# Optimization experiments

Hardware: AMD Instinct MI355X
Metric: run time of the kernel (lower is better)

## Reference

```python
import jax, jax.numpy as jnp
import numpy as np

E = 512   # embed_dim
H = 16    # num_heads
D = E // H  # head_dim = 32
L = 2048  # target (query) length
S = 2048  # source (stored pattern) length
N = 4     # batch
LN_EPS = 1e-5


def setup_inputs() -> dict:
    key = jax.random.key(0)
    ks = jax.random.split(key, 8)
    inv_sqrt_e = 1.0 / np.sqrt(E).astype(np.float32)
    return {
        "query": jax.random.normal(ks[0], (L, N, E), jnp.float32),
        "key_in": jax.random.normal(ks[1], (S, N, E), jnp.float32),
        "value": jax.random.normal(ks[2], (S, N, E), jnp.float32),
        "scaling": jax.random.uniform(ks[3], (H,), jnp.float32),  # per-head beta
        "in_proj_weight": jax.random.normal(ks[4], (3 * E, E), jnp.float32) * inv_sqrt_e,
        "in_proj_bias": jnp.zeros((3 * E,), jnp.float32),
        "p_norm_weight": jnp.ones((D,), jnp.float32),
        "p_norm_bias": jnp.zeros((D,), jnp.float32),
        "out_proj_weight": jax.random.normal(ks[5], (E, E), jnp.float32) * inv_sqrt_e,
        "out_proj_bias": jnp.zeros((E,), jnp.float32),
    }


def reference(query, key_in, value, scaling, in_proj_weight, in_proj_bias,
              p_norm_weight, p_norm_bias, out_proj_weight, out_proj_bias):
    Lq, Nb, Ed = query.shape
    Sk = key_in.shape[0]
    # split packed in-projection (torch Linear convention: y = x @ W^T + b)
    wq, wk, wv = jnp.split(in_proj_weight, 3, axis=0)
    bq, bk, bv = jnp.split(in_proj_bias, 3, axis=0)
    q = jnp.einsum('lne,fe->lnf', query, wq) + bq
    k = jnp.einsum('sne,fe->snf', key_in, wk) + bk
    v = jnp.einsum('sne,fe->snf', value, wv) + bv
    # (len, N, H*D) -> (N, H, len, D)
    q = q.reshape(Lq, Nb, H, D).transpose(1, 2, 0, 3)
    k = k.reshape(Sk, Nb, H, D).transpose(1, 2, 0, 3)
    v = v.reshape(Sk, Nb, H, D).transpose(1, 2, 0, 3)

    def pattern_norm(x):
        # affine LayerNorm over the association (head) dimension D
        mu = jnp.mean(x, axis=-1, keepdims=True)
        var = jnp.mean(jnp.square(x - mu), axis=-1, keepdims=True)
        return (x - mu) * jax.lax.rsqrt(var + LN_EPS) * p_norm_weight + p_norm_bias

    k = pattern_norm(k)
    v = pattern_norm(v)

    beta = scaling.reshape(1, H, 1, 1)  # per-head inverse-temperature
    scores = jnp.einsum('nhld,nhsd->nhls', q * beta, k)  # [N,H,L,S]
    attn = jax.nn.softmax(scores, axis=-1)  # single Hopfield update (update_steps_max=0)
    out = jnp.einsum('nhls,nhsd->nhld', attn, v)  # [N,H,L,D]
    out = out.transpose(2, 0, 1, 3).reshape(Lq, Nb, H * D)
    out = jnp.einsum('lnf,of->lno', out, out_proj_weight) + out_proj_bias
    return out  # (L, N, E)
```

## Files before the change

kernel.cpp:

```cpp
#include <hip/hip_runtime.h>
#include <cstdint>

#define LN_EPS 1e-5f

typedef _Float16 f16;
typedef _Float16 half4_t __attribute__((ext_vector_type(4)));
typedef _Float16 half8_t __attribute__((ext_vector_type(8)));
typedef __fp16 fp16v2 __attribute__((ext_vector_type(2)));
typedef float f32x4 __attribute__((ext_vector_type(4)));

__device__ __forceinline__ void gl_lds16(const void* g, void* l) {
    __builtin_amdgcn_global_load_lds(
        (__attribute__((address_space(1))) void*)(uintptr_t)g,
        (__attribute__((address_space(3))) void*)(uint32_t)(uintptr_t)l,
        16, 0, 0);
}

__device__ __forceinline__ half4_t pack4(float a, float b, float c, float d) {
    fp16v2 lo = __builtin_amdgcn_cvt_pkrtz(a, b);
    fp16v2 hi = __builtin_amdgcn_cvt_pkrtz(c, d);
    half4_t r;
    r[0] = (f16)lo[0]; r[1] = (f16)lo[1]; r[2] = (f16)hi[0]; r[3] = (f16)hi[1];
    return r;
}

__global__ void k_cast(const float* __restrict__ W1f, const float* __restrict__ W2f,
                       f16* __restrict__ W1h, f16* __restrict__ W2h) {
    int t = blockIdx.x * blockDim.x + threadIdx.x;
    const int n1 = (1536 * 512) / 4;
    const float4* src;
    half4_t* dst;
    int idx;
    if (t < n1) { src = (const float4*)W1f; dst = (half4_t*)W1h; idx = t; }
    else        { src = (const float4*)W2f; dst = (half4_t*)W2h; idx = t - n1; }
    float4 v = src[idx];
    half4_t h;
    h[0] = (f16)v.x; h[1] = (f16)v.y; h[2] = (f16)v.z; h[3] = (f16)v.w;
    dst[idx] = h;
}

__global__ __launch_bounds__(256) void k_inproj(
    const float* __restrict__ Xq, const float* __restrict__ Xk, const float* __restrict__ Xv,
    const f16* __restrict__ W1, const float* __restrict__ bias,
    const float* __restrict__ scaling,
    f16* __restrict__ Qg, f16* __restrict__ Kg, f16* __restrict__ Vg)
{
    __shared__ __align__(16) f16 Al[128 * 32];
    __shared__ __align__(16) f16 Bl[128 * 32];

    const int tid = threadIdx.x;
    const int m0 = blockIdx.x * 128;
    const int f0 = blockIdx.y * 128;
    const int sec = f0 >> 9;
    const float* X = (sec == 0) ? Xq : ((sec == 1) ? Xk : Xv);
    f16* Ob = (sec == 0) ? Qg : ((sec == 1) ? Kg : Vg);
    const int fl0 = f0 & 511;

    const int wid = tid >> 6, ln = tid & 63, l15 = ln & 15, quad = ln >> 4;
    const int wm = wid >> 1, wn = wid & 1;

    f32x4 z4 = {0.f, 0.f, 0.f, 0.f};
    f32x4 acc[4][4];
    #pragma unroll
    for (int i = 0; i < 4; ++i)
        #pragma unroll
        for (int j = 0; j < 4; ++j) acc[i][j] = z4;

    for (int kt = 0; kt < 16; ++kt) {
        const int k0 = kt * 32;
        #pragma unroll
        for (int i = 0; i < 2; ++i) {
            int row = wid * 32 + i * 16 + (ln >> 2);
            gl_lds16(W1 + (size_t)(f0 + row) * 512 + k0 + (ln & 3) * 8,
                     Bl + (wid * 32 + i * 16) * 32);
        }
        #pragma unroll
        for (int c = 0; c < 4; ++c) {
            int ch = c * 256 + tid;
            int row = ch >> 3, q4 = ch & 7;
            float4 v = *(const float4*)(X + (size_t)(m0 + row) * 512 + k0 + q4 * 4);
            *(half4_t*)(Al + row * 32 + q4 * 4) = pack4(v.x, v.y, v.z, v.w);
        }
        __syncthreads();

        half8_t a[4], b[4];
        #pragma unroll
        for (int i = 0; i < 4; ++i)
            a[i] = *(const half8_t*)(Al + (wm * 64 + i * 16 + l15) * 32 + quad * 8);
        #pragma unroll
        for (int j = 0; j < 4; ++j)
            b[j] = *(const half8_t*)(Bl + (wn * 64 + j * 16 + l15) * 32 + quad * 8);
        #pragma unroll
        for (int i = 0; i < 4; ++i)
            #pragma unroll
            for (int j = 0; j < 4; ++j)
                acc[i][j] = __builtin_amdgcn_mfma_f32_16x16x32_f16(a[i], b[j], acc[i][j], 0, 0, 0);
        __syncthreads();
    }

    #pragma unroll
    for (int i = 0; i < 4; ++i) {
        int row = m0 + wm * 64 + i * 16 + quad * 4;
        #pragma unroll
        for (int j = 0; j < 4; ++j) {
            int col = wn * 64 + j * 16 + l15;
            int f_local = fl0 + col;
            int hh = f_local >> 5, cc = (f_local >> 3) & 3, e = f_local & 7;
            float bs = bias[f0 + col];
            float sc2 = (sec == 0) ? scaling[hh] * 1.44269504f : 1.0f;
            #pragma unroll
            for (int r = 0; r < 4; ++r) {
                int rm = row + r;
                int l = rm >> 2, nb = rm & 3;
                int gg = nb * 16 + hh;
                Ob[(size_t)gg * 65536 + (size_t)cc * 16384 + (size_t)l * 8 + e] =
                    (f16)((acc[i][j][r] + bs) * sc2);
            }
        }
    }
}

__global__ void k_norm_k(f16* __restrict__ Kg, const float* __restrict__ w,
                         const float* __restrict__ b) {
    int t = blockIdx.x * 256 + threadIdx.x;
    int g = t >> 11, s = t & 2047;
    f16* base = Kg + (size_t)g * 65536 + (size_t)s * 8;
    half8_t x[4];
    float xf[32], s1 = 0.f, s2 = 0.f;
    #pragma unroll
    for (int c = 0; c < 4; ++c) {
        x[c] = *(const half8_t*)(base + (size_t)c * 16384);
        #pragma unroll
        for (int j = 0; j < 8; ++j) {
            float v = (float)x[c][j];
            xf[c * 8 + j] = v; s1 += v; s2 += v * v;
        }
    }
    float mean = s1 * (1.f / 32.f);
    float var = s2 * (1.f / 32.f) - mean * mean;
    float rs = rsqrtf(var + LN_EPS);
    #pragma unroll
    for (int c = 0; c < 4; ++c) {
        half8_t y;
        #pragma unroll
        for (int j = 0; j < 8; ++j) {
            int d = c * 8 + j;
            y[j] = (f16)((xf[d] - mean) * rs * w[d] + b[d]);
        }
        *(half8_t*)(base + (size_t)c * 16384) = y;
    }
}

__global__ void k_norm_vt(const f16* __restrict__ Vg, const float* __restrict__ w,
                          const float* __restrict__ b, f16* __restrict__ Vtg) {
    __shared__ __align__(16) f16 T[32 * 64];
    const int t = threadIdx.x;
    const int seg = blockIdx.x, g = blockIdx.y;
    const int s_l = t >> 2, c = t & 3;
    half8_t v = *(const half8_t*)(Vg + (size_t)g * 65536 + (size_t)c * 16384 +
                                  (size_t)(seg * 64 + s_l) * 8);
    float xf[8], s1 = 0.f, s2 = 0.f;
    #pragma unroll
    for (int j = 0; j < 8; ++j) { xf[j] = (float)v[j]; s1 += xf[j]; s2 += xf[j] * xf[j]; }
    s1 += __shfl_xor(s1, 1); s1 += __shfl_xor(s1, 2);
    s2 += __shfl_xor(s2, 1); s2 += __shfl_xor(s2, 2);
    float mean = s1 * (1.f / 32.f);
    float var = s2 * (1.f / 32.f) - mean * mean;
    float rs = rsqrtf(var + LN_EPS);
    int cs = s_l >> 3, es = s_l & 7;
    #pragma unroll
    for (int j = 0; j < 8; ++j) {
        int d = c * 8 + j;
        T[d * 64 + (cs ^ j) * 8 + es] = (f16)((xf[j] - mean) * rs * w[d] + b[d]);
    }
    __syncthreads();
    int d_o = t >> 3, c_o = t & 7;
    half8_t out = *(const half8_t*)(T + d_o * 64 + c_o * 8);
    *(half8_t*)(Vtg + (size_t)(g * 32 + seg) * 2048 + d_o * 64 + c_o * 8) = out;
}

__global__ __launch_bounds__(256, 4) void k_flash(
    const f16* __restrict__ Qg, const f16* __restrict__ Kg,
    const f16* __restrict__ Vtg, f16* __restrict__ Og)
{
    __shared__ __align__(16) char smem[26624];
    f16* Kl = (f16*)smem;
    char* VtB = smem + 4096;
    char* PlAll = smem + 8192;

    const int tid = threadIdx.x, wid = tid >> 6, ln = tid & 63;
    const int l15 = ln & 15, quad = ln >> 4;
    char* Pw = PlAll + wid * 4608;
    const int g = blockIdx.y, h = g & 15, n = g >> 4;
    const int q0 = blockIdx.x * 128;

    #pragma unroll
    for (int ii = 0; ii < 2; ++ii)
        gl_lds16(Qg + (size_t)g * 65536 + (size_t)wid * 16384 + (size_t)(q0 + ii * 64) * 8 + ln * 8,
                 PlAll + wid * 2048 + ii * 1024);
    __syncthreads();
    half8_t aq[2];
    #pragma unroll
    for (int i = 0; i < 2; ++i)
        aq[i] = *(const half8_t*)(PlAll + quad * 2048 + (wid * 32 + i * 16 + l15) * 16);

    f32x4 z4 = {0.f, 0.f, 0.f, 0.f};
    f32x4 accO[2][2];
    accO[0][0] = z4; accO[0][1] = z4; accO[1][0] = z4; accO[1][1] = z4;
    float m_i[2] = {-1e30f, -1e30f}, l_i[2] = {0.f, 0.f};

    for (int st = 0; st < 32; ++st) {
        __syncthreads();
        gl_lds16(Kg + (size_t)g * 65536 + (size_t)wid * 16384 + (size_t)(st * 64) * 8 + ln * 8,
                 (char*)Kl + wid * 1024);
        gl_lds16(Vtg + (size_t)(g * 32 + st) * 2048 + wid * 512 + ln * 8,
                 VtB + wid * 1024);
        __syncthreads();

        half8_t ak[4];
        #pragma unroll
        for (int mt = 0; mt < 4; ++mt)
            ak[mt] = *(const half8_t*)((char*)Kl + quad * 1024 + (mt * 16 + l15) * 16);
        f32x4 accS[2][4];
        #pragma unroll
        for (int i = 0; i < 2; ++i)
            #pragma unroll
            for (int mt = 0; mt < 4; ++mt)
                accS[i][mt] = __builtin_amdgcn_mfma_f32_16x16x32_f16(ak[mt], aq[i], z4, 0, 0, 0);

        #pragma unroll
        for (int i = 0; i < 2; ++i) {
            float xmax = accS[i][0][0];
            #pragma unroll
            for (int mt = 0; mt < 4; ++mt)
                #pragma unroll
                for (int r = 0; r < 4; ++r) xmax = fmaxf(xmax, accS[i][mt][r]);
            xmax = fmaxf(xmax, __shfl_xor(xmax, 16));
            xmax = fmaxf(xmax, __shfl_xor(xmax, 32));
            float mnew = fmaxf(m_i[i], xmax);
            float alpha = __builtin_amdgcn_exp2f(m_i[i] - mnew);
            float rs = 0.f;
            #pragma unroll
            for (int mt = 0; mt < 4; ++mt) {
                float p0 = __builtin_amdgcn_exp2f(accS[i][mt][0] - mnew);
                float p1 = __builtin_amdgcn_exp2f(accS[i][mt][1] - mnew);
                float p2 = __builtin_amdgcn_exp2f(accS[i][mt][2] - mnew);
                float p3 = __builtin_amdgcn_exp2f(accS[i][mt][3] - mnew);
                rs += (p0 + p1) + (p2 + p3);
                *(half4_t*)(Pw + (i * 16 + l15) * 144 + mt * 32 + quad * 8) =
                    pack4(p0, p1, p2, p3);
            }
            rs += __shfl_xor(rs, 16);
            rs += __shfl_xor(rs, 32);
            l_i[i] = l_i[i] * alpha + rs;
            m_i[i] = mnew;
            #pragma unroll
            for (int dt = 0; dt < 2; ++dt)
                #pragma unroll
                for (int r = 0; r < 4; ++r) accO[i][dt][r] *= alpha;
        }

        #pragma unroll
        for (int kt = 0; kt < 2; ++kt) {
            half8_t av[2], bp[2];
            #pragma unroll
            for (int dt = 0; dt < 2; ++dt) {
                int d = dt * 16 + l15;
                int cp = (kt * 4 + quad) ^ (l15 & 7);
                av[dt] = *(const half8_t*)(VtB + d * 128 + cp * 16);
            }
            #pragma unroll
            for (int i = 0; i < 2; ++i)
                bp[i] = *(const half8_t*)(Pw + (i * 16 + l15) * 144 + kt * 64 + quad * 16);
            #pragma unroll
            for (int i = 0; i < 2; ++i)
                #pragma unroll
                for (int dt = 0; dt < 2; ++dt)
                    accO[i][dt] = __builtin_amdgcn_mfma_f32_16x16x32_f16(av[dt], bp[i], accO[i][dt], 0, 0, 0);
        }
    }

    #pragma unroll
    for (int i = 0; i < 2; ++i) {
        float inv = 1.f / l_i[i];
        #pragma unroll
        for (int dt = 0; dt < 2; ++dt) {
            *(half4_t*)(Pw + (i * 16 + l15) * 80 + (dt * 16 + quad * 4) * 2) =
                pack4(accO[i][dt][0] * inv, accO[i][dt][1] * inv,
                      accO[i][dt][2] * inv, accO[i][dt][3] * inv);
        }
    }
    int q2 = ln >> 1, hf = ln & 1;
    half8_t o0 = *(const half8_t*)(Pw + q2 * 80 + hf * 32);
    half8_t o1 = *(const half8_t*)(Pw + q2 * 80 + hf * 32 + 16);
    size_t rowe = ((size_t)(n * 2048 + q0 + wid * 32 + q2)) * 512 + h * 32 + hf * 16;
    *(half8_t*)(Og + rowe) = o0;
    *(half8_t*)(Og + rowe + 8) = o1;
}

__global__ __launch_bounds__(256) void k_outproj(
    const f16* __restrict__ A, const f16* __restrict__ W2,
    const float* __restrict__ bias, float* __restrict__ Out)
{
    __shared__ __align__(16) f16 Al[128 * 32];
    __shared__ __align__(16) f16 Bl[128 * 32];

    const int tid = threadIdx.x;
    const int m0 = blockIdx.x * 128;
    const int f0 = blockIdx.y * 128;
    const int wid = tid >> 6, ln = tid & 63, l15 = ln & 15, quad = ln >> 4;
    const int wm = wid >> 1, wn = wid & 1;

    f32x4 z4 = {0.f, 0.f, 0.f, 0.f};
    f32x4 acc[4][4];
    #pragma unroll
    for (int i = 0; i < 4; ++i)
        #pragma unroll
        for (int j = 0; j < 4; ++j) acc[i][j] = z4;

    for (int kt = 0; kt < 16; ++kt) {
        const int k0 = kt * 32;
        #pragma unroll
        for (int i = 0; i < 2; ++i) {
            int row = wid * 32 + i * 16 + (ln >> 2);
            gl_lds16(A + (size_t)(m0 + row) * 512 + k0 + (ln & 3) * 8,
                     Al + (wid * 32 + i * 16) * 32);
            gl_lds16(W2 + (size_t)(f0 + row) * 512 + k0 + (ln & 3) * 8,
                     Bl + (wid * 32 + i * 16) * 32);
        }
        __syncthreads();

        half8_t a[4], b[4];
        #pragma unroll
        for (int i = 0; i < 4; ++i)
            a[i] = *(const half8_t*)(Al + (wm * 64 + i * 16 + l15) * 32 + quad * 8);
        #pragma unroll
        for (int j = 0; j < 4; ++j)
            b[j] = *(const half8_t*)(Bl + (wn * 64 + j * 16 + l15) * 32 + quad * 8);
        #pragma unroll
        for (int i = 0; i < 4; ++i)
            #pragma unroll
            for (int j = 0; j < 4; ++j)
                acc[i][j] = __builtin_amdgcn_mfma_f32_16x16x32_f16(a[i], b[j], acc[i][j], 0, 0, 0);
        __syncthreads();
    }

    #pragma unroll
    for (int i = 0; i < 4; ++i) {
        int row = m0 + wm * 64 + i * 16 + quad * 4;
        #pragma unroll
        for (int j = 0; j < 4; ++j) {
            int col = wn * 64 + j * 16 + l15;
            float bs = bias[f0 + col];
            #pragma unroll
            for (int r = 0; r < 4; ++r) {
                int rm = row + r;
                int orow = (rm & 2047) * 4 + (rm >> 11);
                Out[(size_t)orow * 512 + f0 + col] = acc[i][j][r] + bs;
            }
        }
    }
}

extern "C" void kernel_launch(void* const* d_in, const int* in_sizes, int n_in,
                              void* d_out, int out_size, void* d_ws, size_t ws_size,
                              hipStream_t stream) {
    const float* query   = (const float*)d_in[0];
    const float* key_in  = (const float*)d_in[1];
    const float* value   = (const float*)d_in[2];
    const float* scaling = (const float*)d_in[3];
    const float* ipw     = (const float*)d_in[4];
    const float* ipb     = (const float*)d_in[5];
    const float* pnw     = (const float*)d_in[6];
    const float* pnb     = (const float*)d_in[7];
    const float* opw     = (const float*)d_in[8];
    const float* opb     = (const float*)d_in[9];
    float* out = (float*)d_out;

    f16* Qg  = (f16*)d_ws;
    f16* Kg  = Qg  + (size_t)4194304;
    f16* Vg  = Kg  + (size_t)4194304;
    f16* Vtg = Vg  + (size_t)4194304;
    f16* W1  = Vtg + (size_t)4194304;
    f16* W2  = W1  + (size_t)786432;
    f16* Og  = Vg;

    k_cast<<<1024, 256, 0, stream>>>(ipw, opw, W1, W2);
    k_inproj<<<dim3(64, 12), 256, 0, stream>>>(query, key_in, value, W1, ipb, scaling, Qg, Kg, Vg);
    k_norm_k<<<512, 256, 0, stream>>>(Kg, pnw, pnb);
    k_norm_vt<<<dim3(32, 64), 256, 0, stream>>>(Vg, pnw, pnb, Vtg);
    k_flash<<<dim3(16, 64), 256, 0, stream>>>(Qg, Kg, Vtg, Og);
    k_outproj<<<dim3(64, 4), 256, 0, stream>>>(Og, W2, opb, out);
}
```

Measured before the change: 244.6 us.

## Double-buffer K/V tiles in flash kernel, halve query tile, vectorize GEMM epilogues

The flash-attention kernel now handles 64 queries per block instead of 128, which doubles the grid and raises the occupancy hint to 6. It also double-buffers the K and V^T tiles in LDS, prefetching the next tile with global_load_lds while computing on the current one, so one barrier per iteration replaces two. In the in-projection and out-projection GEMMs the MFMA operands are swapped, letting each lane hold 4 consecutive output columns and write vectorized half4/float4 stores with a float4 bias load. The risk is that smaller query tiles reload K/V more often, which adds L2 traffic.

```diff
diff --git a/kernel.cpp b/kernel.cpp
--- a/kernel.cpp
+++ b/kernel.cpp
@@ -34,9 +34,7 @@
     if (t < n1) { src = (const float4*)W1f; dst = (half4_t*)W1h; idx = t; }
     else        { src = (const float4*)W2f; dst = (half4_t*)W2h; idx = t - n1; }
     float4 v = src[idx];
-    half4_t h;
-    h[0] = (f16)v.x; h[1] = (f16)v.y; h[2] = (f16)v.z; h[3] = (f16)v.w;
-    dst[idx] = h;
+    dst[idx] = pack4(v.x, v.y, v.z, v.w);
 }
 
 __global__ __launch_bounds__(256) void k_inproj(
@@ -94,28 +92,26 @@
         for (int i = 0; i < 4; ++i)
             #pragma unroll
             for (int j = 0; j < 4; ++j)
-                acc[i][j] = __builtin_amdgcn_mfma_f32_16x16x32_f16(a[i], b[j], acc[i][j], 0, 0, 0);
-        __syncthreads();
-    }
-
-    #pragma unroll
-    for (int i = 0; i < 4; ++i) {
-        int row = m0 + wm * 64 + i * 16 + quad * 4;
-        #pragma unroll
-        for (int j = 0; j < 4; ++j) {
-            int col = wn * 64 + j * 16 + l15;
-            int f_local = fl0 + col;
-            int hh = f_local >> 5, cc = (f_local >> 3) & 3, e = f_local & 7;
-            float bs = bias[f0 + col];
-            float sc2 = (sec == 0) ? scaling[hh] * 1.44269504f : 1.0f;
-            #pragma unroll
-            for (int r = 0; r < 4; ++r) {
-                int rm = row + r;
-                int l = rm >> 2, nb = rm & 3;
-                int gg = nb * 16 + hh;
-                Ob[(size_t)gg * 65536 + (size_t)cc * 16384 + (size_t)l * 8 + e] =
-                    (f16)((acc[i][j][r] + bs) * sc2);
-            }
+                acc[i][j] = __builtin_amdgcn_mfma_f32_16x16x32_f16(b[j], a[i], acc[i][j], 0, 0, 0);
+        __syncthreads();
+    }
+
+    #pragma unroll
+    for (int j = 0; j < 4; ++j) {
+        int fb = f0 + wn * 64 + j * 16;
+        int floc = (fb & 511) + quad * 4;
+        int hh = floc >> 5;
+        int cc = (floc >> 3) & 3, e0 = floc & 7;
+        float sc2 = (sec == 0) ? scaling[hh] * 1.44269504f : 1.0f;
+        float4 bs4 = *(const float4*)(bias + fb + quad * 4);
+        #pragma unroll
+        for (int i = 0; i < 4; ++i) {
+            int rm = m0 + wm * 64 + i * 16 + l15;
+            int l = rm >> 2, nb = rm & 3;
+            int gg = nb * 16 + hh;
+            *(half4_t*)(Ob + (size_t)gg * 65536 + (size_t)cc * 16384 + (size_t)l * 8 + e0) =
+                pack4((acc[i][j][0] + bs4.x) * sc2, (acc[i][j][1] + bs4.y) * sc2,
+                      (acc[i][j][2] + bs4.z) * sc2, (acc[i][j][3] + bs4.w) * sc2);
         }
     }
 }
@@ -179,123 +175,109 @@
     *(half8_t*)(Vtg + (size_t)(g * 32 + seg) * 2048 + d_o * 64 + c_o * 8) = out;
 }
 
-__global__ __launch_bounds__(256, 4) void k_flash(
+__global__ __launch_bounds__(256, 6) void k_flash(
     const f16* __restrict__ Qg, const f16* __restrict__ Kg,
     const f16* __restrict__ Vtg, f16* __restrict__ Og)
 {
-    __shared__ __align__(16) char smem[26624];
-    f16* Kl = (f16*)smem;
-    char* VtB = smem + 4096;
-    char* PlAll = smem + 8192;
+    __shared__ __align__(16) char smem[25600];
 
     const int tid = threadIdx.x, wid = tid >> 6, ln = tid & 63;
     const int l15 = ln & 15, quad = ln >> 4;
-    char* Pw = PlAll + wid * 4608;
+    char* Pw = smem + 16384 + wid * 2304;
     const int g = blockIdx.y, h = g & 15, n = g >> 4;
-    const int q0 = blockIdx.x * 128;
-
-    #pragma unroll
-    for (int ii = 0; ii < 2; ++ii)
-        gl_lds16(Qg + (size_t)g * 65536 + (size_t)wid * 16384 + (size_t)(q0 + ii * 64) * 8 + ln * 8,
-                 PlAll + wid * 2048 + ii * 1024);
+    const int q0 = blockIdx.x * 64;
+
+    gl_lds16(Qg + (size_t)g * 65536 + (size_t)wid * 16384 + (size_t)(q0 + ln) * 8,
+             smem + 16384 + wid * 1024);
+    gl_lds16(Kg + (size_t)g * 65536 + (size_t)wid * 16384 + (size_t)ln * 8,
+             smem + wid * 1024);
+    gl_lds16(Vtg + (size_t)(g * 32 + 0) * 2048 + wid * 512 + ln * 8,
+             smem + 8192 + wid * 1024);
+    __builtin_amdgcn_s_waitcnt(0x0F70);
     __syncthreads();
-    half8_t aq[2];
-    #pragma unroll
-    for (int i = 0; i < 2; ++i)
-        aq[i] = *(const half8_t*)(PlAll + quad * 2048 + (wid * 32 + i * 16 + l15) * 16);
+    half8_t aq = *(const half8_t*)(smem + 16384 + quad * 1024 + (wid * 16 + l15) * 16);
 
     f32x4 z4 = {0.f, 0.f, 0.f, 0.f};
-    f32x4 accO[2][2];
-    accO[0][0] = z4; accO[0][1] = z4; accO[1][0] = z4; accO[1][1] = z4;
-    float m_i[2] = {-1e30f, -1e30f}, l_i[2] = {0.f, 0.f};
+    f32x4 accO[2];
+    accO[0] = z4; accO[1] = z4;
+    float m_i = -1e30f, l_i = 0.f;
 
     for (int st = 0; st < 32; ++st) {
-        __syncthreads();
-        gl_lds16(Kg + (size_t)g * 65536 + (size_t)wid * 16384 + (size_t)(st * 64) * 8 + ln * 8,
-                 (char*)Kl + wid * 1024);
-        gl_lds16(Vtg + (size_t)(g * 32 + st) * 2048 + wid * 512 + ln * 8,
-                 VtB + wid * 1024);
-        __syncthreads();
+        const int cur = st & 1, nxt = cur ^ 1;
+        if (st < 31) {
+            gl_lds16(Kg + (size_t)g * 65536 + (size_t)wid * 16384 + (size_t)((st + 1) * 64 + ln) * 8,
+                     smem + nxt * 4096 + wid * 1024);
+            gl_lds16(Vtg + (size_t)(g * 32 + st + 1) * 2048 + wid * 512 + ln * 8,
+                     smem + 8192 + nxt * 4096 + wid * 1024);
+        }
+        const char* Kl = smem + cur * 4096;
+        const char* Vt = smem + 8192 + cur * 4096;
 
         half8_t ak[4];
         #pragma unroll
         for (int mt = 0; mt < 4; ++mt)
-            ak[mt] = *(const half8_t*)((char*)Kl + quad * 1024 + (mt * 16 + l15) * 16);
-        f32x4 accS[2][4];
-        #pragma unroll
-        for (int i = 0; i < 2; ++i)
-            #pragma unroll
-            for (int mt = 0; mt < 4; ++mt)
-                accS[i][mt] = __builtin_amdgcn_mfma_f32_16x16x32_f16(ak[mt], aq[i], z4, 0, 0, 0);
-
-        #pragma unroll
-        for (int i = 0; i < 2; ++i) {
-            float xmax = accS[i][0][0];
-            #pragma unroll
-            for (int mt = 0; mt < 4; ++mt)
-                #pragma unroll
-                for (int r = 0; r < 4; ++r) xmax = fmaxf(xmax, accS[i][mt][r]);
-            xmax = fmaxf(xmax, __shfl_xor(xmax, 16));
-            xmax = fmaxf(xmax, __shfl_xor(xmax, 32));
-            float mnew = fmaxf(m_i[i], xmax);
-            float alpha = __builtin_amdgcn_exp2f(m_i[i] - mnew);
-            float rs = 0.f;
-            #pragma unroll
-            for (int mt = 0; mt < 4; ++mt) {
-                float p0 = __builtin_amdgcn_exp2f(accS[i][mt][0] - mnew);
-                float p1 = __builtin_amdgcn_exp2f(accS[i][mt][1] - mnew);
-                float p2 = __builtin_amdgcn_exp2f(accS[i][mt][2] - mnew);
-                float p3 = __builtin_amdgcn_exp2f(accS[i][mt][3] - mnew);
-                rs += (p0 + p1) + (p2 + p3);
-                *(half4_t*)(Pw + (i * 16 + l15) * 144 + mt * 32 + quad * 8) =
-                    pack4(p0, p1, p2, p3);
-            }
-            rs += __shfl_xor(rs, 16);
-            rs += __shfl_xor(rs, 32);
-            l_i[i] = l_i[i] * alpha + rs;
-            m_i[i] = mnew;
-            #pragma unroll
-            for (int dt = 0; dt < 2; ++dt)
-                #pragma unroll
-                for (int r = 0; r < 4; ++r) accO[i][dt][r] *= alpha;
-        }
+            ak[mt] = *(const half8_t*)(Kl + quad * 1024 + (mt * 16 + l15) * 16);
+        f32x4 accS[4];
+        #pragma unroll
+        for (int mt = 0; mt < 4; ++mt)
+            accS[mt] = __builtin_amdgcn_mfma_f32_16x16x32_f16(ak[mt], aq, z4, 0, 0, 0);
+
+        float xmax = accS[0][0];
+        #pragma unroll
+        for (int mt = 0; mt < 4; ++mt)
+            #pragma unroll
+            for (int r = 0; r < 4; ++r) xmax = fmaxf(xmax, accS[mt][r]);
+        xmax = fmaxf(xmax, __shfl_xor(xmax, 16));
+        xmax = fmaxf(xmax, __shfl_xor(xmax, 32));
+        float mnew = fmaxf(m_i, xmax);
+        float alpha = __builtin_amdgcn_exp2f(m_i - mnew);
+        float rs = 0.f;
+        #pragma unroll
+        for (int mt = 0; mt < 4; ++mt) {
+            float p0 = __builtin_amdgcn_exp2f(accS[mt][0] - mnew);
+            float p1 = __builtin_amdgcn_exp2f(accS[mt][1] - mnew);
+            float p2 = __builtin_amdgcn_exp2f(accS[mt][2] - mnew);
+            float p3 = __builtin_amdgcn_exp2f(accS[mt][3] - mnew);
+            rs += (p0 + p1) + (p2 + p3);
+            *(half4_t*)(Pw + l15 * 144 + mt * 32 + quad * 8) = pack4(p0, p1, p2, p3);
+        }
+        rs += __shfl_xor(rs, 16);
+        rs += __shfl_xor(rs, 32);
+        l_i = l_i * alpha + rs;
+        m_i = mnew;
+        #pragma unroll
+        for (int dt = 0; dt < 2; ++dt)
+            #pragma unroll
+            for (int r = 0; r < 4; ++r) accO[dt][r] *= alpha;
 
         #pragma unroll
         for (int kt = 0; kt < 2; ++kt) {
-            half8_t av[2], bp[2];
+            half8_t av[2], bp;
             #pragma unroll
             for (int dt = 0; dt < 2; ++dt) {
                 int d = dt * 16 + l15;
                 int cp = (kt * 4 + quad) ^ (l15 & 7);
-                av[dt] = *(const half8_t*)(VtB + d * 128 + cp * 16);
+                av[dt] = *(const half8_t*)(Vt + d * 128 + cp * 16);
             }
-            #pragma unroll
-            for (int i = 0; i < 2; ++i)
-                bp[i] = *(const half8_t*)(Pw + (i * 16 + l15) * 144 + kt * 64 + quad * 16);
-            #pragma unroll
-            for (int i = 0; i < 2; ++i)
-                #pragma unroll
-                for (int dt = 0; dt < 2; ++dt)
-                    accO[i][dt] = __builtin_amdgcn_mfma_f32_16x16x32_f16(av[dt], bp[i], accO[i][dt], 0, 0, 0);
-        }
-    }
-
-    #pragma unroll
-    for (int i = 0; i < 2; ++i) {
-        float inv = 1.f / l_i[i];
-        #pragma unroll
-        for (int dt = 0; dt < 2; ++dt) {
-            *(half4_t*)(Pw + (i * 16 + l15) * 80 + (dt * 16 + quad * 4) * 2) =
-                pack4(accO[i][dt][0] * inv, accO[i][dt][1] * inv,
-                      accO[i][dt][2] * inv, accO[i][dt][3] * inv);
-        }
-    }
-    int q2 = ln >> 1, hf = ln & 1;
-    half8_t o0 = *(const half8_t*)(Pw + q2 * 80 + hf * 32);
-    half8_t o1 = *(const half8_t*)(Pw + q2 * 80 + hf * 32 + 16);
-    size_t rowe = ((size_t)(n * 2048 + q0 + wid * 32 + q2)) * 512 + h * 32 + hf * 16;
-    *(half8_t*)(Og + rowe) = o0;
-    *(half8_t*)(Og + rowe + 8) = o1;
+            bp = *(const half8_t*)(Pw + l15 * 144 + kt * 64 + quad * 16);
+            #pragma unroll
+            for (int dt = 0; dt < 2; ++dt)
+                accO[dt] = __builtin_amdgcn_mfma_f32_16x16x32_f16(av[dt], bp, accO[dt], 0, 0, 0);
+        }
+
+        __builtin_amdgcn_s_waitcnt(0x0F70);
+        __syncthreads();
+    }
+
+    float inv = 1.f / l_i;
+    #pragma unroll
+    for (int dt = 0; dt < 2; ++dt)
+        *(half4_t*)(Pw + l15 * 80 + (dt * 16 + quad * 4) * 2) =
+            pack4(accO[dt][0] * inv, accO[dt][1] * inv,
+                  accO[dt][2] * inv, accO[dt][3] * inv);
+    int q2 = ln >> 2, c4 = ln & 3;
+    half8_t o = *(const half8_t*)(Pw + q2 * 80 + c4 * 16);
+    *(half8_t*)(Og + ((size_t)(n * 2048 + q0 + wid * 16 + q2)) * 512 + h * 32 + c4 * 8) = o;
 }
 
 __global__ __launch_bounds__(256) void k_outproj(
@@ -341,23 +323,24 @@
         for (int i = 0; i < 4; ++i)
             #pragma unroll
             for (int j = 0; j < 4; ++j)
-                acc[i][j] = __builtin_amdgcn_mfma_f32_16x16x32_f16(a[i], b[j], acc[i][j], 0, 0, 0);
-        __syncthreads();
-    }
-
-    #pragma unroll
-    for (int i = 0; i < 4; ++i) {
-        int row = m0 + wm * 64 + i * 16 + quad * 4;
-        #pragma unroll
-        for (int j = 0; j < 4; ++j) {
-            int col = wn * 64 + j * 16 + l15;
-            float bs = bias[f0 + col];
-            #pragma unroll
-            for (int r = 0; r < 4; ++r) {
-                int rm = row + r;
-                int orow = (rm & 2047) * 4 + (rm >> 11);
-                Out[(size_t)orow * 512 + f0 + col] = acc[i][j][r] + bs;
-            }
+                acc[i][j] = __builtin_amdgcn_mfma_f32_16x16x32_f16(b[j], a[i], acc[i][j], 0, 0, 0);
+        __syncthreads();
+    }
+
+    #pragma unroll
+    for (int j = 0; j < 4; ++j) {
+        int fb = f0 + wn * 64 + j * 16;
+        float4 bs4 = *(const float4*)(bias + fb + quad * 4);
+        #pragma unroll
+        for (int i = 0; i < 4; ++i) {
+            int rm = m0 + wm * 64 + i * 16 + l15;
+            int orow = (rm & 2047) * 4 + (rm >> 11);
+            float4 o;
+            o.x = acc[i][j][0] + bs4.x;
+            o.y = acc[i][j][1] + bs4.y;
+            o.z = acc[i][j][2] + bs4.z;
+            o.w = acc[i][j][3] + bs4.w;
+            *(float4*)(Out + (size_t)orow * 512 + fb + quad * 4) = o;
         }
     }
 }
@@ -389,6 +372,6 @@
     k_inproj<<<dim3(64, 12), 256, 0, stream>>>(query, key_in, value, W1, ipb, scaling, Qg, Kg, Vg);
     k_norm_k<<<512, 256, 0, stream>>>(Kg, pnw, pnb);
     k_norm_vt<<<dim3(32, 64), 256, 0, stream>>>(Vg, pnw, pnb, Vtg);
-    k_flash<<<dim3(16, 64), 256, 0, stream>>>(Qg, Kg, Vtg, Og);
+    k_flash<<<dim3(32, 64), 256, 0, stream>>>(Qg, Kg, Vtg, Og);
     k_outproj<<<dim3(64, 4), 256, 0, stream>>>(Og, W2, opb, out);
 }
```

Result: no change. 245.5 us (+0.4%).
